# Performance work log

Hardware: AMD Instinct MI355X
Metric: run time of the kernel (lower is better)

Reference implementation:

```python
import jax, jax.numpy as jnp
import numpy as np

OUT_SIZE, EMB, DEC_H, ENC_D = 172, 128, 256, 256
B, L = 256, 1024


def setup_inputs() -> dict:
    key = jax.random.key(0)
    ks = jax.random.split(key, 16)
    s = lambda k, shp, scale=0.05: (jax.random.normal(k, shp, dtype=jnp.float32) * scale)
    return {
        "h0": jax.random.normal(ks[0], (B, DEC_H), dtype=jnp.float32),
        "c0": jax.random.normal(ks[1], (B, DEC_H), dtype=jnp.float32),
        "o_t": jax.random.normal(ks[2], (B, DEC_H), dtype=jnp.float32),
        "enc_out": jax.random.normal(ks[3], (B, L, ENC_D), dtype=jnp.float32),
        "lasttarget": jax.random.randint(ks[4], (B, 1), 0, OUT_SIZE),
        # learned params
        "emb": s(ks[5], (OUT_SIZE, EMB), 1.0),
        "W_ih": s(ks[6], (4 * DEC_H, DEC_H + EMB)),
        "W_hh": s(ks[7], (4 * DEC_H, DEC_H)),
        "b_ih": s(ks[8], (4 * DEC_H,)),
        "b_hh": s(ks[9], (4 * DEC_H,)),
        "W1": s(ks[10], (ENC_D, ENC_D)),
        "W2": s(ks[11], (ENC_D, DEC_H)),
        "W3": s(ks[12], (DEC_H, DEC_H + ENC_D)),
        "W_out": s(ks[13], (OUT_SIZE, DEC_H)),
        "beta": jax.random.uniform(ks[14], (ENC_D,), dtype=jnp.float32, minval=-0.01, maxval=0.01),
    }


def reference(h0, c0, o_t, enc_out, lasttarget, emb, W_ih, W_hh, b_ih, b_hh, W1, W2, W3, W_out, beta):
    # embedding + concat -> LSTMCell input (B, DEC_H+EMB)
    prev_y = emb[lasttarget[:, 0]]              # (B, EMB)
    inp = jnp.concatenate([prev_y, o_t], axis=1)
    # LSTMCell: gate order i, f, g, o (PyTorch convention)
    gates = inp @ W_ih.T + b_ih + h0 @ W_hh.T + b_hh   # (B, 4*DEC_H)
    i, f, g, o = jnp.split(gates, 4, axis=1)
    c_t = jax.nn.sigmoid(f) * c0 + jax.nn.sigmoid(i) * jnp.tanh(g)
    h_t = jax.nn.sigmoid(o) * jnp.tanh(c_t)
    # additive attention over enc positions
    alpha = jnp.tanh(enc_out @ W1.T + (h_t @ W2.T)[:, None, :])  # (B, L, ENC_D)
    scores = jnp.sum(beta * alpha, axis=-1)                      # (B, L)
    attn = jax.nn.softmax(scores, axis=-1)
    context = jnp.einsum("bl,bld->bd", attn, enc_out)            # (B, ENC_D)
    # output projection
    o_new = jnp.tanh(jnp.concatenate([h_t, context], axis=1) @ W3.T)  # (B, DEC_H)
    logit = jax.nn.softmax(o_new @ W_out.T, axis=1)                   # (B, OUT_SIZE)
    return (h_t, c_t, o_new, logit)
```

## Files before the change

### kernel.cpp

```cpp
#include <hip/hip_runtime.h>

#define B_   256
#define L_   1024
#define H_   256
#define EMB_ 128
#define OUT_ 172

typedef float f32x4 __attribute__((ext_vector_type(4)));
typedef __bf16 bf16x8 __attribute__((ext_vector_type(8)));
typedef unsigned short us8 __attribute__((ext_vector_type(8)));

static __device__ __forceinline__ unsigned short f2bf(float f) {
    unsigned u = __float_as_uint(f);
    u += 0x7fffu + ((u >> 16) & 1u);
    return (unsigned short)(u >> 16);
}
static __device__ __forceinline__ float bf2f(unsigned short s) {
    return __uint_as_float(((unsigned)s) << 16);
}
static __device__ __forceinline__ us8 cvt8(const float* __restrict__ p) {
    float4 x0 = *(const float4*)p, x1 = *(const float4*)(p + 4);
    us8 v;
    v[0]=f2bf(x0.x); v[1]=f2bf(x0.y); v[2]=f2bf(x0.z); v[3]=f2bf(x0.w);
    v[4]=f2bf(x1.x); v[5]=f2bf(x1.y); v[6]=f2bf(x1.z); v[7]=f2bf(x1.w);
    return v;
}
static __device__ __forceinline__ float tanh_fast(float x) {
    float e = __expf(2.f * x);
    return 1.f - 2.f * __builtin_amdgcn_rcpf(e + 1.f);
}
static __device__ __forceinline__ float sigm_fast(float x) {
    return __builtin_amdgcn_rcpf(1.f + __expf(-x));
}

#define TS 40

__global__ __launch_bounds__(256) void k_gates(
    const float* __restrict__ h0, const float* __restrict__ o_t,
    const int* __restrict__ lasttarget, const float* __restrict__ emb,
    const float* __restrict__ W_ih, const float* __restrict__ W_hh,
    const float* __restrict__ b_ih, const float* __restrict__ b_hh,
    float* __restrict__ gates)
{
    const int m0 = (blockIdx.x >> 4) * 64;
    const int n0 = (blockIdx.x & 15) * 64;
    const int tid = threadIdx.x;
    const int w = tid >> 6, lane = tid & 63, quad = lane >> 4, l15 = lane & 15;

    __shared__ __align__(16) unsigned short As[64 * TS];
    __shared__ __align__(16) unsigned short Bs[64 * TS];

    float bias[4];
    #pragma unroll
    for (int nt = 0; nt < 4; nt++) {
        int n = n0 + nt * 16 + l15;
        bias[nt] = b_ih[n] + b_hh[n];
    }

    f32x4 acc[4] = {{0,0,0,0},{0,0,0,0},{0,0,0,0},{0,0,0,0}};
    const int sm = tid >> 2, sk8 = (tid & 3) * 8;
    const int lt = lasttarget[m0 + sm];

    for (int kc = 0; kc < 20; kc++) {
        const int k = kc * 32 + sk8;
        const float* ap;
        if (k < 128)      ap = emb + lt * EMB_ + k;
        else if (k < 384) ap = o_t + (m0 + sm) * H_ + (k - 128);
        else              ap = h0  + (m0 + sm) * H_ + (k - 384);
        *(us8*)&As[sm * TS + sk8] = cvt8(ap);
        const int j = n0 + sm;
        const float* bp = (k < 384) ? (W_ih + j * 384 + k) : (W_hh + j * 256 + (k - 384));
        *(us8*)&Bs[sm * TS + sk8] = cvt8(bp);
        __syncthreads();
        bf16x8 a = __builtin_bit_cast(bf16x8, *(const us8*)&As[(w * 16 + l15) * TS + quad * 8]);
        #pragma unroll
        for (int nt = 0; nt < 4; nt++) {
            bf16x8 b = __builtin_bit_cast(bf16x8, *(const us8*)&Bs[(nt * 16 + l15) * TS + quad * 8]);
            acc[nt] = __builtin_amdgcn_mfma_f32_16x16x32_bf16(a, b, acc[nt], 0, 0, 0);
        }
        __syncthreads();
    }
    #pragma unroll
    for (int nt = 0; nt < 4; nt++)
        #pragma unroll
        for (int r = 0; r < 4; r++)
            gates[(m0 + w * 16 + quad * 4 + r) * 1024 + n0 + nt * 16 + l15] = acc[nt][r] + bias[nt];
}

__global__ __launch_bounds__(256) void k_lstm(
    const float* __restrict__ gates, const float* __restrict__ c0,
    float* __restrict__ out, unsigned short* __restrict__ A3u)
{
    const int b = blockIdx.x, t = threadIdx.x;
    const float* g = gates + b * 1024;
    float gi = g[t], gf = g[256 + t], gg = g[512 + t], go = g[768 + t];
    float c = sigm_fast(gf) * c0[b * H_ + t] + sigm_fast(gi) * tanh_fast(gg);
    float h = sigm_fast(go) * tanh_fast(c);
    out[b * H_ + t]           = h;
    out[B_ * H_ + b * H_ + t] = c;
    A3u[b * 256 + t] = f2bf(h);
}

__global__ __launch_bounds__(256) void k_hw2(
    const unsigned short* __restrict__ A3u, const float* __restrict__ W2,
    float* __restrict__ hW2)
{
    const int m0 = (blockIdx.x >> 2) * 64;
    const int n0 = (blockIdx.x & 3) * 64;
    const int tid = threadIdx.x;
    const int w = tid >> 6, lane = tid & 63, quad = lane >> 4, l15 = lane & 15;
    __shared__ __align__(16) unsigned short As[64 * TS];
    __shared__ __align__(16) unsigned short Bs[64 * TS];
    f32x4 acc[4] = {{0,0,0,0},{0,0,0,0},{0,0,0,0},{0,0,0,0}};
    const int sm = tid >> 2, sk8 = (tid & 3) * 8;
    for (int kc = 0; kc < 8; kc++) {
        const int k = kc * 32 + sk8;
        *(us8*)&As[sm * TS + sk8] = *(const us8*)&A3u[(m0 + sm) * 256 + k];
        *(us8*)&Bs[sm * TS + sk8] = cvt8(W2 + (n0 + sm) * 256 + k);
        __syncthreads();
        bf16x8 a = __builtin_bit_cast(bf16x8, *(const us8*)&As[(w * 16 + l15) * TS + quad * 8]);
        #pragma unroll
        for (int nt = 0; nt < 4; nt++) {
            bf16x8 b = __builtin_bit_cast(bf16x8, *(const us8*)&Bs[(nt * 16 + l15) * TS + quad * 8]);
            acc[nt] = __builtin_amdgcn_mfma_f32_16x16x32_bf16(a, b, acc[nt], 0, 0, 0);
        }
        __syncthreads();
    }
    #pragma unroll
    for (int nt = 0; nt < 4; nt++)
        #pragma unroll
        for (int r = 0; r < 4; r++)
            hW2[(m0 + w * 16 + quad * 4 + r) * 256 + n0 + nt * 16 + l15] = acc[nt][r];
}

#define ROWSTR 264

__global__ __launch_bounds__(512, 2) void k_attn(
    const float* __restrict__ enc, const float* __restrict__ W1,
    const float* __restrict__ hW2, const float* __restrict__ beta,
    float* __restrict__ ctx_part, float* __restrict__ s_part)
{
    const int blk = blockIdx.x;
    const int b = blk >> 1, half = blk & 1;
    const int tid = threadIdx.x;
    const int wave = tid >> 6, lane = tid & 63;
    const int quad = lane >> 4, l15 = lane & 15;

    __shared__ __align__(16) unsigned short encs[3][16 * ROWSTR];
    __shared__ float sp[2][8][16];
    __shared__ float wexp[2][16];
    __shared__ float2 cr[512];

    bf16x8 wf[8][2];
    float hw2v[2], betav[2];
    #pragma unroll
    for (int nt = 0; nt < 2; nt++) {
        int n = wave * 32 + nt * 16 + l15;
        hw2v[nt]  = hW2[b * H_ + n];
        betav[nt] = beta[n];
        #pragma unroll
        for (int ks = 0; ks < 8; ks++)
            wf[ks][nt] = __builtin_bit_cast(bf16x8, cvt8(W1 + n * 256 + ks * 32 + quad * 8));
    }

    const float* encb = enc + ((size_t)b * L_ + half * 512) * H_;
    const int srow = tid >> 5, scol = (tid & 31) * 8;

    *(us8*)&encs[0][srow * ROWSTR + scol] = cvt8(encb + srow * 256 + scol);
    float4 x0, x1;
    {
        const float* p = encb + 16 * 256 + srow * 256 + scol;
        x0 = *(const float4*)p; x1 = *(const float4*)(p + 4);
    }
    __syncthreads();

    const int cp = tid & 127, q = tid >> 7;
    float2 ctx2 = {0.f, 0.f};
    float ssum = 0.f;

    for (int it = 0; it < 32; it++) {
        const int cur = it % 3;
        const int nxt = (it + 1) % 3;
        const int par = it & 1;
        float4 y0 = {0,0,0,0}, y1 = {0,0,0,0};
        if (it < 30) {
            const float* p = encb + (it + 2) * 16 * 256 + srow * 256 + scol;
            y0 = *(const float4*)p; y1 = *(const float4*)(p + 4);
        }
        f32x4 acc0 = {0,0,0,0}, acc1 = {0,0,0,0};
        const unsigned short* arow = &encs[cur][l15 * ROWSTR + quad * 8];
        #pragma unroll
        for (int ks = 0; ks < 8; ks++) {
            bf16x8 a = __builtin_bit_cast(bf16x8, *(const us8*)(arow + ks * 32));
            acc0 = __builtin_amdgcn_mfma_f32_16x16x32_bf16(a, wf[ks][0], acc0, 0, 0, 0);
            acc1 = __builtin_amdgcn_mfma_f32_16x16x32_bf16(a, wf[ks][1], acc1, 0, 0, 0);
        }
        if (it < 31) {
            us8 v;
            v[0]=f2bf(x0.x); v[1]=f2bf(x0.y); v[2]=f2bf(x0.z); v[3]=f2bf(x0.w);
            v[4]=f2bf(x1.x); v[5]=f2bf(x1.y); v[6]=f2bf(x1.z); v[7]=f2bf(x1.w);
            *(us8*)&encs[nxt][srow * ROWSTR + scol] = v;
        }
        float p4[4];
        #pragma unroll
        for (int r = 0; r < 4; r++) {
            float t0 = tanh_fast(acc0[r] + hw2v[0]);
            float t1 = tanh_fast(acc1[r] + hw2v[1]);
            p4[r] = betav[0] * t0 + betav[1] * t1;
        }
        #pragma unroll
        for (int m = 1; m < 16; m <<= 1) {
            p4[0] += __shfl_xor(p4[0], m);
            p4[1] += __shfl_xor(p4[1], m);
            p4[2] += __shfl_xor(p4[2], m);
            p4[3] += __shfl_xor(p4[3], m);
        }
        if (l15 == 0) {
            #pragma unroll
            for (int r = 0; r < 4; r++) sp[par][wave][quad * 4 + r] = p4[r];
        }
        __syncthreads();
        if (tid < 16) {
            float sc = sp[par][0][tid] + sp[par][1][tid] + sp[par][2][tid] + sp[par][3][tid]
                     + sp[par][4][tid] + sp[par][5][tid] + sp[par][6][tid] + sp[par][7][tid];
            wexp[par][tid] = __expf(sc);
        }
        __syncthreads();
        {
            const unsigned* base = (const unsigned*)&encs[cur][0];
            float cx = ctx2.x, cy = ctx2.y;
            #pragma unroll
            for (int r = 0; r < 4; r++) {
                const int row = q * 4 + r;
                unsigned u = base[row * (ROWSTR / 2) + cp];
                float wv = wexp[par][row];
                cx += wv * __uint_as_float(u << 16);
                cy += wv * __uint_as_float(u & 0xffff0000u);
            }
            ctx2.x = cx; ctx2.y = cy;
        }
        if (tid == 0) {
            float s2 = 0.f;
            #pragma unroll
            for (int r = 0; r < 16; r++) s2 += wexp[par][r];
            ssum += s2;
        }
        x0 = y0; x1 = y1;
    }
    cr[tid] = ctx2;
    __syncthreads();
    if (tid == 0) s_part[blk] = ssum;
    if (tid < 128) {
        float2 a0 = cr[tid], a1 = cr[tid + 128], a2 = cr[tid + 256], a3 = cr[tid + 384];
        float2 o;
        o.x = a0.x + a1.x + a2.x + a3.x;
        o.y = a0.y + a1.y + a2.y + a3.y;
        ((float2*)ctx_part)[blk * 128 + tid] = o;
    }
}

__global__ __launch_bounds__(256) void k_out3(
    const unsigned short* __restrict__ A3u, const float* __restrict__ ctx_part,
    const float* __restrict__ s_part, const float* __restrict__ W3,
    float* __restrict__ out, unsigned short* __restrict__ A4u)
{
    const int m0 = (blockIdx.x >> 2) * 64;
    const int n0 = (blockIdx.x & 3) * 64;
    const int tid = threadIdx.x;
    const int w = tid >> 6, lane = tid & 63, quad = lane >> 4, l15 = lane & 15;
    __shared__ __align__(16) unsigned short As[64 * TS];
    __shared__ __align__(16) unsigned short Bs[64 * TS];
    f32x4 acc[4] = {{0,0,0,0},{0,0,0,0},{0,0,0,0},{0,0,0,0}};
    const int sm = tid >> 2, sk8 = (tid & 3) * 8;
    const int bb = m0 + sm;
    const float inv = 1.f / (s_part[2 * bb] + s_part[2 * bb + 1]);
    for (int kc = 0; kc < 16; kc++) {
        const int k = kc * 32 + sk8;
        if (k < 256) {
            *(us8*)&As[sm * TS + sk8] = *(const us8*)&A3u[bb * 256 + k];
        } else {
            const int c = k - 256;
            const float* p0 = ctx_part + (size_t)(2 * bb) * 256 + c;
            const float* p1 = ctx_part + (size_t)(2 * bb + 1) * 256 + c;
            float4 a0 = *(const float4*)p0, a1 = *(const float4*)(p0 + 4);
            float4 b0 = *(const float4*)p1, b1 = *(const float4*)(p1 + 4);
            us8 v;
            v[0]=f2bf((a0.x+b0.x)*inv); v[1]=f2bf((a0.y+b0.y)*inv);
            v[2]=f2bf((a0.z+b0.z)*inv); v[3]=f2bf((a0.w+b0.w)*inv);
            v[4]=f2bf((a1.x+b1.x)*inv); v[5]=f2bf((a1.y+b1.y)*inv);
            v[6]=f2bf((a1.z+b1.z)*inv); v[7]=f2bf((a1.w+b1.w)*inv);
            *(us8*)&As[sm * TS + sk8] = v;
        }
        *(us8*)&Bs[sm * TS + sk8] = cvt8(W3 + (n0 + sm) * 512 + k);
        __syncthreads();
        bf16x8 a = __builtin_bit_cast(bf16x8, *(const us8*)&As[(w * 16 + l15) * TS + quad * 8]);
        #pragma unroll
        for (int nt = 0; nt < 4; nt++) {
            bf16x8 b = __builtin_bit_cast(bf16x8, *(const us8*)&Bs[(nt * 16 + l15) * TS + quad * 8]);
            acc[nt] = __builtin_amdgcn_mfma_f32_16x16x32_bf16(a, b, acc[nt], 0, 0, 0);
        }
        __syncthreads();
    }
    #pragma unroll
    for (int nt = 0; nt < 4; nt++)
        #pragma unroll
        for (int r = 0; r < 4; r++) {
            int row = m0 + w * 16 + quad * 4 + r, col = n0 + nt * 16 + l15;
            float o = tanh_fast(acc[nt][r]);
            out[2 * B_ * H_ + row * 256 + col] = o;
            A4u[row * 256 + col] = f2bf(o);
        }
}

__global__ __launch_bounds__(256) void k_logit(
    const unsigned short* __restrict__ A4u, const float* __restrict__ W_out,
    float* __restrict__ out)
{
    const int m0 = blockIdx.x * 64;
    const int tid = threadIdx.x;
    const int w = tid >> 6, lane = tid & 63, quad = lane >> 4, l15 = lane & 15;
    __shared__ __align__(16) unsigned short As[64 * TS];
    __shared__ __align__(16) unsigned short Bs[192 * TS];
    __shared__ float lg[64][196];
    f32x4 acc[12];
    #pragma unroll
    for (int nt = 0; nt < 12; nt++) acc[nt] = (f32x4){0,0,0,0};
    const int sm = tid >> 2, sk8 = (tid & 3) * 8;
    for (int kc = 0; kc < 8; kc++) {
        const int k = kc * 32 + sk8;
        *(us8*)&As[sm * TS + sk8] = *(const us8*)&A4u[(m0 + sm) * 256 + k];
        #pragma unroll
        for (int rr = 0; rr < 3; rr++) {
            int j = rr * 64 + sm;
            us8 v = {0,0,0,0,0,0,0,0};
            if (j < OUT_) v = cvt8(W_out + j * 256 + k);
            *(us8*)&Bs[j * TS + sk8] = v;
        }
        __syncthreads();
        bf16x8 a = __builtin_bit_cast(bf16x8, *(const us8*)&As[(w * 16 + l15) * TS + quad * 8]);
        #pragma unroll
        for (int nt = 0; nt < 12; nt++) {
            bf16x8 b = __builtin_bit_cast(bf16x8, *(const us8*)&Bs[(nt * 16 + l15) * TS + quad * 8]);
            acc[nt] = __builtin_amdgcn_mfma_f32_16x16x32_bf16(a, b, acc[nt], 0, 0, 0);
        }
        __syncthreads();
    }
    #pragma unroll
    for (int nt = 0; nt < 12; nt++)
        #pragma unroll
        for (int r = 0; r < 4; r++)
            lg[w * 16 + quad * 4 + r][nt * 16 + l15] = acc[nt][r];
    __syncthreads();
    const int m = tid >> 2, p = tid & 3;
    const int cb = p * 43;
    float mx = -1e30f;
    for (int c = 0; c < 43; c++) mx = fmaxf(mx, lg[m][cb + c]);
    mx = fmaxf(mx, __shfl_xor(mx, 1));
    mx = fmaxf(mx, __shfl_xor(mx, 2));
    float s = 0.f;
    for (int c = 0; c < 43; c++) { float e = __expf(lg[m][cb + c] - mx); lg[m][cb + c] = e; s += e; }
    s += __shfl_xor(s, 1);
    s += __shfl_xor(s, 2);
    float inv = 1.f / s;
    for (int c = 0; c < 43; c++)
        out[3 * B_ * H_ + (m0 + m) * OUT_ + cb + c] = lg[m][cb + c] * inv;
}

extern "C" void kernel_launch(void* const* d_in, const int* in_sizes, int n_in,
                              void* d_out, int out_size, void* d_ws, size_t ws_size,
                              hipStream_t stream)
{
    const float* h0   = (const float*)d_in[0];
    const float* c0   = (const float*)d_in[1];
    const float* o_t  = (const float*)d_in[2];
    const float* enc  = (const float*)d_in[3];
    const int*   lt   = (const int*)  d_in[4];
    const float* emb  = (const float*)d_in[5];
    const float* W_ih = (const float*)d_in[6];
    const float* W_hh = (const float*)d_in[7];
    const float* b_ih = (const float*)d_in[8];
    const float* b_hh = (const float*)d_in[9];
    const float* W1   = (const float*)d_in[10];
    const float* W2   = (const float*)d_in[11];
    const float* W3   = (const float*)d_in[12];
    const float* Wo   = (const float*)d_in[13];
    const float* beta = (const float*)d_in[14];
    float* out = (float*)d_out;
    float* ws  = (float*)d_ws;

    float*          gates    = ws;
    float*          hW2      = ws + 262144;
    float*          ctx_part = ws + 327680;
    float*          s_part   = ws + 458752;
    unsigned short* A3u      = (unsigned short*)(ws + 459264);
    unsigned short* A4u      = (unsigned short*)(ws + 492032);

    k_gates<<<64, 256, 0, stream>>>(h0, o_t, lt, emb, W_ih, W_hh, b_ih, b_hh, gates);
    k_lstm <<<256, 256, 0, stream>>>(gates, c0, out, A3u);
    k_hw2  <<<16, 256, 0, stream>>>(A3u, W2, hW2);
    k_attn <<<512, 512, 0, stream>>>(enc, W1, hW2, beta, ctx_part, s_part);
    k_out3 <<<16, 256, 0, stream>>>(A3u, ctx_part, s_part, W3, out, A4u);
    k_logit<<<4, 256, 0, stream>>>(A4u, Wo, out);
}
```

Before: 464.3 us.

## Software-pipeline attention loop with one barrier per step and fuse hW2 into LSTM

The attention loop now staggers the score MFMA, the exp/score reduction and the context accumulation across three consecutive iterations. It uses a 4-deep LDS ring, so each step needs a single __syncthreads instead of two. The separate h·W2 GEMM kernel is removed and computed as an fp32 dot product inside k_lstm, saving one launch but having every block re-read all of W2. The bf16 conversions also switch to the native __bf16 cast, which the compiler can lower to hardware conversion instructions.

```diff
diff --git a/kernel.cpp b/kernel.cpp
--- a/kernel.cpp
+++ b/kernel.cpp
@@ -11,19 +11,15 @@
 typedef unsigned short us8 __attribute__((ext_vector_type(8)));
 
 static __device__ __forceinline__ unsigned short f2bf(float f) {
-    unsigned u = __float_as_uint(f);
-    u += 0x7fffu + ((u >> 16) & 1u);
-    return (unsigned short)(u >> 16);
-}
-static __device__ __forceinline__ float bf2f(unsigned short s) {
-    return __uint_as_float(((unsigned)s) << 16);
+    __bf16 h = (__bf16)f;
+    return __builtin_bit_cast(unsigned short, h);
 }
 static __device__ __forceinline__ us8 cvt8(const float* __restrict__ p) {
     float4 x0 = *(const float4*)p, x1 = *(const float4*)(p + 4);
-    us8 v;
-    v[0]=f2bf(x0.x); v[1]=f2bf(x0.y); v[2]=f2bf(x0.z); v[3]=f2bf(x0.w);
-    v[4]=f2bf(x1.x); v[5]=f2bf(x1.y); v[6]=f2bf(x1.z); v[7]=f2bf(x1.w);
-    return v;
+    bf16x8 v;
+    v[0]=(__bf16)x0.x; v[1]=(__bf16)x0.y; v[2]=(__bf16)x0.z; v[3]=(__bf16)x0.w;
+    v[4]=(__bf16)x1.x; v[5]=(__bf16)x1.y; v[6]=(__bf16)x1.z; v[7]=(__bf16)x1.w;
+    return __builtin_bit_cast(us8, v);
 }
 static __device__ __forceinline__ float tanh_fast(float x) {
     float e = __expf(2.f * x);
@@ -89,7 +85,9 @@
 
 __global__ __launch_bounds__(256) void k_lstm(
     const float* __restrict__ gates, const float* __restrict__ c0,
-    float* __restrict__ out, unsigned short* __restrict__ A3u)
+    const float* __restrict__ W2,
+    float* __restrict__ out, unsigned short* __restrict__ A3u,
+    float* __restrict__ hW2)
 {
     const int b = blockIdx.x, t = threadIdx.x;
     const float* g = gates + b * 1024;
@@ -99,38 +97,20 @@
     out[b * H_ + t]           = h;
     out[B_ * H_ + b * H_ + t] = c;
     A3u[b * 256 + t] = f2bf(h);
-}
-
-__global__ __launch_bounds__(256) void k_hw2(
-    const unsigned short* __restrict__ A3u, const float* __restrict__ W2,
-    float* __restrict__ hW2)
-{
-    const int m0 = (blockIdx.x >> 2) * 64;
-    const int n0 = (blockIdx.x & 3) * 64;
-    const int tid = threadIdx.x;
-    const int w = tid >> 6, lane = tid & 63, quad = lane >> 4, l15 = lane & 15;
-    __shared__ __align__(16) unsigned short As[64 * TS];
-    __shared__ __align__(16) unsigned short Bs[64 * TS];
-    f32x4 acc[4] = {{0,0,0,0},{0,0,0,0},{0,0,0,0},{0,0,0,0}};
-    const int sm = tid >> 2, sk8 = (tid & 3) * 8;
-    for (int kc = 0; kc < 8; kc++) {
-        const int k = kc * 32 + sk8;
-        *(us8*)&As[sm * TS + sk8] = *(const us8*)&A3u[(m0 + sm) * 256 + k];
-        *(us8*)&Bs[sm * TS + sk8] = cvt8(W2 + (n0 + sm) * 256 + k);
-        __syncthreads();
-        bf16x8 a = __builtin_bit_cast(bf16x8, *(const us8*)&As[(w * 16 + l15) * TS + quad * 8]);
-        #pragma unroll
-        for (int nt = 0; nt < 4; nt++) {
-            bf16x8 b = __builtin_bit_cast(bf16x8, *(const us8*)&Bs[(nt * 16 + l15) * TS + quad * 8]);
-            acc[nt] = __builtin_amdgcn_mfma_f32_16x16x32_bf16(a, b, acc[nt], 0, 0, 0);
-        }
-        __syncthreads();
-    }
-    #pragma unroll
-    for (int nt = 0; nt < 4; nt++)
-        #pragma unroll
-        for (int r = 0; r < 4; r++)
-            hW2[(m0 + w * 16 + quad * 4 + r) * 256 + n0 + nt * 16 + l15] = acc[nt][r];
+
+    __shared__ float hs[256];
+    hs[t] = h;
+    __syncthreads();
+    float acc = 0.f;
+    const float* w2r = W2 + t * 256;
+    #pragma unroll 4
+    for (int k = 0; k < 256; k += 8) {
+        float4 wa = *(const float4*)(w2r + k);
+        float4 wb = *(const float4*)(w2r + k + 4);
+        acc += hs[k]*wa.x + hs[k+1]*wa.y + hs[k+2]*wa.z + hs[k+3]*wa.w
+             + hs[k+4]*wb.x + hs[k+5]*wb.y + hs[k+6]*wb.z + hs[k+7]*wb.w;
+    }
+    hW2[b * 256 + t] = acc;
 }
 
 #define ROWSTR 264
@@ -146,7 +126,7 @@
     const int wave = tid >> 6, lane = tid & 63;
     const int quad = lane >> 4, l15 = lane & 15;
 
-    __shared__ __align__(16) unsigned short encs[3][16 * ROWSTR];
+    __shared__ __align__(16) unsigned short encs[4][16 * ROWSTR];
     __shared__ float sp[2][8][16];
     __shared__ float wexp[2][16];
     __shared__ float2 cr[512];
@@ -178,73 +158,73 @@
     float2 ctx2 = {0.f, 0.f};
     float ssum = 0.f;
 
-    for (int it = 0; it < 32; it++) {
-        const int cur = it % 3;
-        const int nxt = (it + 1) % 3;
-        const int par = it & 1;
+    for (int it = 0; it < 34; it++) {
         float4 y0 = {0,0,0,0}, y1 = {0,0,0,0};
         if (it < 30) {
-            const float* p = encb + (it + 2) * 16 * 256 + srow * 256 + scol;
+            const float* p = encb + (size_t)(it + 2) * 16 * 256 + srow * 256 + scol;
             y0 = *(const float4*)p; y1 = *(const float4*)(p + 4);
         }
-        f32x4 acc0 = {0,0,0,0}, acc1 = {0,0,0,0};
-        const unsigned short* arow = &encs[cur][l15 * ROWSTR + quad * 8];
-        #pragma unroll
-        for (int ks = 0; ks < 8; ks++) {
-            bf16x8 a = __builtin_bit_cast(bf16x8, *(const us8*)(arow + ks * 32));
-            acc0 = __builtin_amdgcn_mfma_f32_16x16x32_bf16(a, wf[ks][0], acc0, 0, 0, 0);
-            acc1 = __builtin_amdgcn_mfma_f32_16x16x32_bf16(a, wf[ks][1], acc1, 0, 0, 0);
-        }
-        if (it < 31) {
-            us8 v;
-            v[0]=f2bf(x0.x); v[1]=f2bf(x0.y); v[2]=f2bf(x0.z); v[3]=f2bf(x0.w);
-            v[4]=f2bf(x1.x); v[5]=f2bf(x1.y); v[6]=f2bf(x1.z); v[7]=f2bf(x1.w);
-            *(us8*)&encs[nxt][srow * ROWSTR + scol] = v;
-        }
-        float p4[4];
-        #pragma unroll
-        for (int r = 0; r < 4; r++) {
-            float t0 = tanh_fast(acc0[r] + hw2v[0]);
-            float t1 = tanh_fast(acc1[r] + hw2v[1]);
-            p4[r] = betav[0] * t0 + betav[1] * t1;
-        }
-        #pragma unroll
-        for (int m = 1; m < 16; m <<= 1) {
-            p4[0] += __shfl_xor(p4[0], m);
-            p4[1] += __shfl_xor(p4[1], m);
-            p4[2] += __shfl_xor(p4[2], m);
-            p4[3] += __shfl_xor(p4[3], m);
-        }
-        if (l15 == 0) {
-            #pragma unroll
-            for (int r = 0; r < 4; r++) sp[par][wave][quad * 4 + r] = p4[r];
-        }
-        __syncthreads();
-        if (tid < 16) {
-            float sc = sp[par][0][tid] + sp[par][1][tid] + sp[par][2][tid] + sp[par][3][tid]
-                     + sp[par][4][tid] + sp[par][5][tid] + sp[par][6][tid] + sp[par][7][tid];
-            wexp[par][tid] = __expf(sc);
-        }
-        __syncthreads();
-        {
-            const unsigned* base = (const unsigned*)&encs[cur][0];
+        if (it >= 1 && it <= 32 && tid < 16) {
+            const int pp = (it - 1) & 1;
+            float sc = sp[pp][0][tid] + sp[pp][1][tid] + sp[pp][2][tid] + sp[pp][3][tid]
+                     + sp[pp][4][tid] + sp[pp][5][tid] + sp[pp][6][tid] + sp[pp][7][tid];
+            wexp[pp][tid] = __expf(sc);
+        }
+        if (it >= 2) {
+            const int pb = (it - 2) & 3, pp = (it - 2) & 1;
+            const unsigned* base = (const unsigned*)&encs[pb][0];
             float cx = ctx2.x, cy = ctx2.y;
             #pragma unroll
             for (int r = 0; r < 4; r++) {
                 const int row = q * 4 + r;
                 unsigned u = base[row * (ROWSTR / 2) + cp];
-                float wv = wexp[par][row];
+                float wv = wexp[pp][row];
                 cx += wv * __uint_as_float(u << 16);
                 cy += wv * __uint_as_float(u & 0xffff0000u);
             }
             ctx2.x = cx; ctx2.y = cy;
-        }
-        if (tid == 0) {
-            float s2 = 0.f;
+            if (tid == 0) {
+                float s2 = 0.f;
+                #pragma unroll
+                for (int r = 0; r < 16; r++) s2 += wexp[pp][r];
+                ssum += s2;
+            }
+        }
+        if (it < 32) {
+            f32x4 acc0 = {0,0,0,0}, acc1 = {0,0,0,0};
+            const unsigned short* arow = &encs[it & 3][l15 * ROWSTR + quad * 8];
             #pragma unroll
-            for (int r = 0; r < 16; r++) s2 += wexp[par][r];
-            ssum += s2;
-        }
+            for (int ks = 0; ks < 8; ks++) {
+                bf16x8 a = __builtin_bit_cast(bf16x8, *(const us8*)(arow + ks * 32));
+                acc0 = __builtin_amdgcn_mfma_f32_16x16x32_bf16(a, wf[ks][0], acc0, 0, 0, 0);
+                acc1 = __builtin_amdgcn_mfma_f32_16x16x32_bf16(a, wf[ks][1], acc1, 0, 0, 0);
+            }
+            float p4[4];
+            #pragma unroll
+            for (int r = 0; r < 4; r++) {
+                float t0 = tanh_fast(acc0[r] + hw2v[0]);
+                float t1 = tanh_fast(acc1[r] + hw2v[1]);
+                p4[r] = betav[0] * t0 + betav[1] * t1;
+            }
+            #pragma unroll
+            for (int m = 1; m < 16; m <<= 1) {
+                p4[0] += __shfl_xor(p4[0], m);
+                p4[1] += __shfl_xor(p4[1], m);
+                p4[2] += __shfl_xor(p4[2], m);
+                p4[3] += __shfl_xor(p4[3], m);
+            }
+            if (l15 == 0) {
+                #pragma unroll
+                for (int r = 0; r < 4; r++) sp[it & 1][wave][quad * 4 + r] = p4[r];
+            }
+        }
+        if (it < 31) {
+            bf16x8 v;
+            v[0]=(__bf16)x0.x; v[1]=(__bf16)x0.y; v[2]=(__bf16)x0.z; v[3]=(__bf16)x0.w;
+            v[4]=(__bf16)x1.x; v[5]=(__bf16)x1.y; v[6]=(__bf16)x1.z; v[7]=(__bf16)x1.w;
+            *(us8*)&encs[(it + 1) & 3][srow * ROWSTR + scol] = __builtin_bit_cast(us8, v);
+        }
+        __syncthreads();
         x0 = y0; x1 = y1;
     }
     cr[tid] = ctx2;
@@ -284,12 +264,12 @@
             const float* p1 = ctx_part + (size_t)(2 * bb + 1) * 256 + c;
             float4 a0 = *(const float4*)p0, a1 = *(const float4*)(p0 + 4);
             float4 b0 = *(const float4*)p1, b1 = *(const float4*)(p1 + 4);
-            us8 v;
-            v[0]=f2bf((a0.x+b0.x)*inv); v[1]=f2bf((a0.y+b0.y)*inv);
-            v[2]=f2bf((a0.z+b0.z)*inv); v[3]=f2bf((a0.w+b0.w)*inv);
-            v[4]=f2bf((a1.x+b1.x)*inv); v[5]=f2bf((a1.y+b1.y)*inv);
-            v[6]=f2bf((a1.z+b1.z)*inv); v[7]=f2bf((a1.w+b1.w)*inv);
-            *(us8*)&As[sm * TS + sk8] = v;
+            bf16x8 v;
+            v[0]=(__bf16)((a0.x+b0.x)*inv); v[1]=(__bf16)((a0.y+b0.y)*inv);
+            v[2]=(__bf16)((a0.z+b0.z)*inv); v[3]=(__bf16)((a0.w+b0.w)*inv);
+            v[4]=(__bf16)((a1.x+b1.x)*inv); v[5]=(__bf16)((a1.y+b1.y)*inv);
+            v[6]=(__bf16)((a1.z+b1.z)*inv); v[7]=(__bf16)((a1.w+b1.w)*inv);
+            *(us8*)&As[sm * TS + sk8] = __builtin_bit_cast(us8, v);
         }
         *(us8*)&Bs[sm * TS + sk8] = cvt8(W3 + (n0 + sm) * 512 + k);
         __syncthreads();
@@ -396,8 +376,7 @@
     unsigned short* A4u      = (unsigned short*)(ws + 492032);
 
     k_gates<<<64, 256, 0, stream>>>(h0, o_t, lt, emb, W_ih, W_hh, b_ih, b_hh, gates);
-    k_lstm <<<256, 256, 0, stream>>>(gates, c0, out, A3u);
-    k_hw2  <<<16, 256, 0, stream>>>(A3u, W2, hW2);
+    k_lstm <<<256, 256, 0, stream>>>(gates, c0, W2, out, A3u, hW2);
     k_attn <<<512, 512, 0, stream>>>(enc, W1, hW2, beta, ctx_part, s_part);
     k_out3 <<<16, 256, 0, stream>>>(A3u, ctx_part, s_part, W3, out, A4u);
     k_logit<<<4, 256, 0, stream>>>(A4u, Wo, out);
```

Result: no change. 463.8 us (-0.1%).
